# Kernel optimization log

Measured on AMD Instinct MI355X. Metric: run time of the kernel, lower is better.

## Reference

```python
import jax, jax.numpy as jnp
import numpy as np
from jax import lax

DIM = 192
HEADS = 8
EPS = 1e-5


def setup_inputs() -> dict:
    key = jax.random.key(0)
    ks = jax.random.split(key, 8)
    B, C, H, W = 1, DIM, 64, 64
    x = jax.random.normal(ks[0], (B, C, H, W), dtype=jnp.float32)
    gamma = jnp.ones((C,), dtype=jnp.float32)
    beta = jnp.zeros((C,), dtype=jnp.float32)
    w_qkv = jax.random.normal(ks[1], (3 * C, C), dtype=jnp.float32) * (1.0 / np.sqrt(C))
    # depthwise 3x3 conv: (out_ch=3C, in_ch/groups=1, 3, 3), bias present (Conv2d default)
    w_dw = jax.random.normal(ks[2], (3 * C, 1, 3, 3), dtype=jnp.float32) * (1.0 / 3.0)
    b_dw = jax.random.normal(ks[3], (3 * C,), dtype=jnp.float32) * 0.01
    w_proj = jax.random.normal(ks[4], (C, C), dtype=jnp.float32) * (1.0 / np.sqrt(C))
    temperature = jnp.ones((HEADS, 1, 1), dtype=jnp.float32)
    return {"x": x, "gamma": gamma, "beta": beta, "w_qkv": w_qkv,
            "w_dw": w_dw, "b_dw": b_dw, "w_proj": w_proj,
            "temperature": temperature}


def _mdta(x, gamma, beta, w_qkv, w_dw, b_dw, w_proj, temperature):
    B, C, H, W = x.shape
    heads = HEADS
    d = C // heads
    N = H * W
    # LayerNorm over channel dim (applied on NHWC permute in torch)
    mean = jnp.mean(x, axis=1, keepdims=True)
    var = jnp.var(x, axis=1, keepdims=True)
    x_ln = (x - mean) * lax.rsqrt(var + EPS)
    x_ln = x_ln * gamma[None, :, None, None] + beta[None, :, None, None]
    # 1x1 conv (no bias): [B,3C,H,W]
    qkv = jnp.einsum('oc,bchw->bohw', w_qkv, x_ln)
    # depthwise 3x3 conv, padding=1, groups=3C
    qkv = lax.conv_general_dilated(
        qkv, w_dw, window_strides=(1, 1), padding=((1, 1), (1, 1)),
        dimension_numbers=('NCHW', 'OIHW', 'NCHW'),
        feature_group_count=3 * C)
    qkv = qkv + b_dw[None, :, None, None]
    q, k, v = jnp.split(qkv, 3, axis=1)
    q = q.reshape(B, heads, d, N)
    k = k.reshape(B, heads, d, N)
    v = v.reshape(B, heads, d, N)
    # attn[b,h,n,m] = sum_d q[b,h,d,n] k[b,h,d,m], scaled by learnable temperature
    attn = jnp.einsum('bhdn,bhdm->bhnm', q, k) * temperature  # (heads,1,1) broadcasts
    attn = jax.nn.softmax(attn, axis=-1)
    # out[b,h,d,n] = sum_m attn[b,h,n,m] v[b,h,d,m]
    out = jnp.einsum('bhnm,bhdm->bhdn', attn, v)
    out = out.reshape(B, C, H, W)
    out = jnp.einsum('oc,bchw->bohw', w_proj, out)
    return out + x


def reference(x, gamma, beta, w_qkv, w_dw, b_dw, w_proj, temperature):
    return _mdta(x, gamma, beta, w_qkv, w_dw, b_dw, w_proj, temperature)
```

## Files before the change

kernel.cpp:

```cpp
#include <hip/hip_runtime.h>
#include <hip/hip_bf16.h>


typedef __bf16 bf16;
typedef __bf16 bf16x2 __attribute__((ext_vector_type(2)));
typedef __bf16 bf16x4 __attribute__((ext_vector_type(4)));
typedef __bf16 bf16x8 __attribute__((ext_vector_type(8)));
typedef float f32x4 __attribute__((ext_vector_type(4)));

#define C_DIM 192
#define N_PIX 4096
#define HEADS 8
#define DHEAD 24
#define DPAD 32
#define C3 576
#define NSPLIT 8

__device__ inline float fast_exp2(float x) {
#if __has_builtin(__builtin_amdgcn_exp2f)
    return __builtin_amdgcn_exp2f(x);
#else
    return exp2f(x);
#endif
}

__device__ inline f32x4 mfma16(bf16x8 a, bf16x8 b, f32x4 c) {
    return __builtin_amdgcn_mfma_f32_16x16x32_bf16(a, b, c, 0, 0, 0);
}

__global__ __launch_bounds__(256) void prep_ln(const float* __restrict__ x,
                                               const float* __restrict__ gamma,
                                               const float* __restrict__ beta,
                                               bf16* __restrict__ xln_t,
                                               const float* __restrict__ wqkv,
                                               const float* __restrict__ wproj,
                                               bf16* __restrict__ wqkv_b,
                                               bf16* __restrict__ wproj_b,
                                               float* __restrict__ maxk2) {
    int b = blockIdx.x, t = threadIdx.x;
    if (b >= 256) {
        int idx = (b - 256) * 256 + t;
        if (idx < C3 * C_DIM) wqkv_b[idx] = (bf16)wqkv[idx];
        if (idx < C_DIM * C_DIM) wproj_b[idx] = (bf16)wproj[idx];
        if (b == 256 && t < 8) maxk2[t] = 0.0f;
        return;
    }
    __shared__ float sred[256], ssred[256];
    int pixg = t & 15, cg = t >> 4;
    int p = b * 16 + pixg;
    float v[12];
    float s = 0.f, ss = 0.f;
    for (int j = 0; j < 12; ++j) {
        float f = x[(cg * 12 + j) * N_PIX + p];
        v[j] = f; s += f; ss += f * f;
    }
    sred[t] = s; ssred[t] = ss;
    __syncthreads();
    float S = 0.f, SS = 0.f;
    for (int k = 0; k < 16; ++k) { S += sred[k * 16 + pixg]; SS += ssred[k * 16 + pixg]; }
    float mean = S * (1.0f / C_DIM);
    float var = SS * (1.0f / C_DIM) - mean * mean;
    float rstd = rsqrtf(var + 1e-5f);
    for (int g = 0; g < 3; ++g) {
        bf16x4 w;
        for (int j = 0; j < 4; ++j) {
            int c = cg * 12 + g * 4 + j;
            w[j] = (bf16)((v[g * 4 + j] - mean) * rstd * gamma[c] + beta[c]);
        }
        *(bf16x4*)(xln_t + p * C_DIM + cg * 12 + g * 4) = w;
    }
}

__global__ __launch_bounds__(256) void gemm192(const bf16* __restrict__ A,
                                               const bf16* __restrict__ BT,
                                               bf16* __restrict__ outb) {
    const int K = 192;
    int n0 = blockIdx.x * 64;
    int m0 = blockIdx.y * 64;
    int tid = threadIdx.x;
    int wave = tid >> 6, lane = tid & 63;
    int l16 = lane & 15, quad = lane >> 4;
    int wm = (wave >> 1) * 32, wn = (wave & 1) * 32;
    f32x4 acc[2][2] = {};
    for (int kk = 0; kk < K; kk += 32) {
        bf16x8 a0 = *(const bf16x8*)(A + (m0 + wm + l16) * K + kk + quad * 8);
        bf16x8 a1 = *(const bf16x8*)(A + (m0 + wm + 16 + l16) * K + kk + quad * 8);
        bf16x8 b0 = *(const bf16x8*)(BT + (n0 + wn + l16) * K + kk + quad * 8);
        bf16x8 b1 = *(const bf16x8*)(BT + (n0 + wn + 16 + l16) * K + kk + quad * 8);
        acc[0][0] = mfma16(a0, b0, acc[0][0]);
        acc[0][1] = mfma16(a0, b1, acc[0][1]);
        acc[1][0] = mfma16(a1, b0, acc[1][0]);
        acc[1][1] = mfma16(a1, b1, acc[1][1]);
    }
    for (int i = 0; i < 2; ++i)
        for (int j = 0; j < 2; ++j)
            for (int r = 0; r < 4; ++r) {
                int row = m0 + wm + i * 16 + quad * 4 + r;
                int col = n0 + wn + j * 16 + l16;
                outb[row * N_PIX + col] = (bf16)acc[i][j][r];
            }
}

__global__ __launch_bounds__(256) void gemm_proj(const bf16* __restrict__ A,
                                                 const bf16* __restrict__ BT,
                                                 float* __restrict__ outf,
                                                 const float* __restrict__ resid) {
    const int K = 192;
    int n0 = blockIdx.x * 32;
    int m0 = blockIdx.y * 64;
    int tid = threadIdx.x;
    int wave = tid >> 6, lane = tid & 63;
    int l16 = lane & 15, quad = lane >> 4;
    int mrow = m0 + wave * 16;
    float rv[8];
    for (int j = 0; j < 2; ++j)
        for (int r = 0; r < 4; ++r)
            rv[j * 4 + r] = resid[(size_t)(mrow + quad * 4 + r) * N_PIX + n0 + j * 16 + l16];
    f32x4 acc[2] = {};
    for (int kk = 0; kk < K; kk += 32) {
        bf16x8 a = *(const bf16x8*)(A + (mrow + l16) * K + kk + quad * 8);
        bf16x8 b0 = *(const bf16x8*)(BT + (n0 + l16) * K + kk + quad * 8);
        bf16x8 b1 = *(const bf16x8*)(BT + (n0 + 16 + l16) * K + kk + quad * 8);
        acc[0] = mfma16(a, b0, acc[0]);
        acc[1] = mfma16(a, b1, acc[1]);
    }
    for (int j = 0; j < 2; ++j)
        for (int r = 0; r < 4; ++r) {
            int row = mrow + quad * 4 + r;
            int col = n0 + j * 16 + l16;
            outf[(size_t)row * N_PIX + col] = acc[j][r] + rv[j * 4 + r];
        }
}

__global__ __launch_bounds__(256) void dwconv(const bf16* __restrict__ qkv,
                                              const float* __restrict__ wdw,
                                              const float* __restrict__ bdw,
                                              bf16* __restrict__ qt,
                                              bf16* __restrict__ kt,
                                              bf16* __restrict__ vl,
                                              float* __restrict__ maxk2) {
    __shared__ float k2s[24][64];
    int bx = blockIdx.x;
    int part = bx >> 9;
    int h = (bx >> 6) & 7;
    int y = bx & 63;
    int t = threadIdx.x;
    int ch_local = t >> 3;
    int seg = t & 7;
    int px0 = seg * 8;
    bool active = ch_local < 24;

    float acc[8];
    if (active) {
        int ch = part * C_DIM + h * DHEAD + ch_local;
        const bf16* in = qkv + (size_t)ch * N_PIX;
        float w[9];
        for (int i = 0; i < 9; ++i) w[i] = wdw[ch * 9 + i];
        float bias = bdw[ch];
        float rowv[3][10];
        for (int r = 0; r < 3; ++r) {
            int yy = y + r - 1;
            if (yy >= 0 && yy < 64) {
                bf16x8 v8 = *(const bf16x8*)(in + yy * 64 + px0);
                for (int j = 0; j < 8; ++j) rowv[r][j + 1] = (float)v8[j];
                rowv[r][0] = (seg > 0) ? (float)in[yy * 64 + px0 - 1] : 0.f;
                rowv[r][9] = (seg < 7) ? (float)in[yy * 64 + px0 + 8] : 0.f;
            } else {
                for (int j = 0; j < 10; ++j) rowv[r][j] = 0.f;
            }
        }
        for (int j = 0; j < 8; ++j) {
            float a = bias;
            for (int r = 0; r < 3; ++r)
                a += w[r * 3 + 0] * rowv[r][j] + w[r * 3 + 1] * rowv[r][j + 1]
                   + w[r * 3 + 2] * rowv[r][j + 2];
            acc[j] = a;
        }
    }

    if (part == 2) {
        if (active) {
            bf16x8 v8;
            for (int j = 0; j < 8; ++j) v8[j] = (bf16)acc[j];
            *(bf16x8*)(vl + ((size_t)(h * DPAD + ch_local)) * N_PIX + y * 64 + px0) = v8;
        } else {
            int i = t - 192;
            int dd = 24 + (i >> 3);
            int s2 = i & 7;
            bf16 val = (bf16)((dd == 24) ? 1.0f : 0.0f);
            bf16x8 v8;
            for (int j = 0; j < 8; ++j) v8[j] = val;
            *(bf16x8*)(vl + ((size_t)(h * DPAD + dd)) * N_PIX + y * 64 + s2 * 8) = v8;
        }
    } else {
        bf16* dst = (part == 0 ? qt : kt) + ((size_t)h * N_PIX + y * 64) * DPAD;
        if (active) {
            for (int j = 0; j < 8; ++j)
                dst[(size_t)(px0 + j) * DPAD + ch_local] = (bf16)acc[j];
        } else {
            int i = t - 192;
            bf16x8 z;
            for (int j = 0; j < 8; ++j) z[j] = (bf16)0.0f;
            *(bf16x8*)(dst + (size_t)i * DPAD + 24) = z;
        }
        if (part == 1) {
            if (active)
                for (int j = 0; j < 8; ++j) k2s[ch_local][px0 + j] = acc[j] * acc[j];
            __syncthreads();
            if (t < 64) {
                float s = 0.f;
                for (int c = 0; c < 24; ++c) s += k2s[c][t];
                for (int off = 1; off < 64; off <<= 1)
                    s = fmaxf(s, __shfl_xor(s, off, 64));
                if (t == 0) atomicMax((unsigned int*)(maxk2 + h), __float_as_uint(s));
            }
        }
    }
}

__global__ __launch_bounds__(256, 4) void flash_attn(const bf16* __restrict__ qt,
                                                     const bf16* __restrict__ kt,
                                                     const bf16* __restrict__ vl,
                                                     const float* __restrict__ temp,
                                                     const float* __restrict__ maxk2,
                                                     bf16* __restrict__ opart,
                                                     bf16* __restrict__ lpart) {
    __shared__ __align__(16) bf16 Plds[4 * 4096];

    int tid = threadIdx.x;
    int wave = tid >> 6, lane = tid & 63;
    int l16 = lane & 15, quad = lane >> 4;
    int head = blockIdx.x & 7;
    int qb = (blockIdx.x >> 3) & 15;
    int split = blockIdx.x >> 7;
    int nbase = qb * 256 + wave * 64;
    float tl = temp[head] * 1.44269504f;

    const bf16* qrow = qt + ((size_t)head * N_PIX + nbase) * DPAD;
    bf16x8 aq[4];
    for (int f = 0; f < 4; ++f)
        aq[f] = *(const bf16x8*)(qrow + (size_t)(f * 16 + l16) * DPAD + quad * 8);

    float mk2 = maxk2[head];
    float Bb[4];
    for (int f = 0; f < 4; ++f) {
        float q2 = 0.f;
        for (int j = 0; j < 8; ++j) { float v = (float)aq[f][j]; q2 += v * v; }
        q2 += __shfl_xor(q2, 16, 64);
        q2 += __shfl_xor(q2, 32, 64);
        Bb[f] = fabsf(tl) * sqrtf(q2 * mk2) + 1.0f;
    }

    const bf16* kbase = kt + (size_t)head * N_PIX * DPAD;
    const bf16* vbase = vl + (size_t)head * DPAD * N_PIX;
    bf16* pw = Plds + wave * 4096;

    f32x4 o0[4] = {}, o1[4] = {};

    #pragma unroll 2
    for (int it = 0; it < 64 / NSPLIT; ++it) {
        int m0 = (split * (64 / NSPLIT) + it) * 64;
        bf16x8 ak[4];
        for (int mt = 0; mt < 4; ++mt)
            ak[mt] = *(const bf16x8*)(kbase + (size_t)(m0 + mt * 16 + l16) * DPAD + quad * 8);
        bf16x8 av[4];
        av[0] = *(const bf16x8*)(vbase + (size_t)l16 * N_PIX + m0 + quad * 8);
        av[1] = *(const bf16x8*)(vbase + (size_t)(16 + l16) * N_PIX + m0 + quad * 8);
        av[2] = *(const bf16x8*)(vbase + (size_t)l16 * N_PIX + m0 + 32 + quad * 8);
        av[3] = *(const bf16x8*)(vbase + (size_t)(16 + l16) * N_PIX + m0 + 32 + quad * 8);

        for (int f = 0; f < 4; ++f) {
            f32x4 z = {0.f, 0.f, 0.f, 0.f};
            f32x4 st[4];
            for (int mt = 0; mt < 4; ++mt) st[mt] = mfma16(ak[mt], aq[f], z);
            for (int mt = 0; mt < 4; ++mt) {
                bf16x4 pk;
                for (int r = 0; r < 4; ++r)
                    pk[r] = (bf16)fast_exp2(__builtin_fmaf(st[mt][r], tl, -Bb[f]));
                int chunk = mt * 2 + (quad >> 1);
                *(bf16x4*)(pw + f * 1024 + (chunk * 16 + l16) * 8 + (quad & 1) * 4) = pk;
            }
        }
        for (int f = 0; f < 4; ++f) {
            bf16x8 ap0 = *(const bf16x8*)(pw + f * 1024 + (quad * 16 + l16) * 8);
            bf16x8 ap1 = *(const bf16x8*)(pw + f * 1024 + ((4 + quad) * 16 + l16) * 8);
            o0[f] = mfma16(av[0], ap0, o0[f]);
            o1[f] = mfma16(av[1], ap0, o1[f]);
            o0[f] = mfma16(av[2], ap1, o0[f]);
            o1[f] = mfma16(av[3], ap1, o1[f]);
        }
    }

    for (int f = 0; f < 4; ++f) {
        int n = nbase + f * 16 + l16;
        size_t rowo = ((size_t)(split * 8 + head) * N_PIX + n) * 24;
        bf16x4 w0;
        for (int r = 0; r < 4; ++r) w0[r] = (bf16)o0[f][r];
        *(bf16x4*)(opart + rowo + quad * 4) = w0;
        if (quad < 2) {
            bf16x4 w1;
            for (int r = 0; r < 4; ++r) w1[r] = (bf16)o1[f][r];
            *(bf16x4*)(opart + rowo + 16 + quad * 4) = w1;
        }
        if (quad == 2)
            lpart[(size_t)(split * 8 + head) * N_PIX + n] = (bf16)o1[f][0];
    }
}

__global__ __launch_bounds__(256) void combine(const bf16* __restrict__ opart,
                                               const bf16* __restrict__ lpart,
                                               bf16* __restrict__ outt) {
    int idx = blockIdx.x * 256 + threadIdx.x;
    int n = idx & 4095;
    int h = idx >> 12;
    float acc[24];
    for (int j = 0; j < 24; ++j) acc[j] = 0.f;
    float l = 0.f;
    for (int s = 0; s < NSPLIT; ++s) {
        const bf16* row = opart + ((size_t)(s * 8 + h) * N_PIX + n) * 24;
        bf16x8 a = *(const bf16x8*)(row);
        bf16x8 b = *(const bf16x8*)(row + 8);
        bf16x8 c = *(const bf16x8*)(row + 16);
        for (int j = 0; j < 8; ++j) {
            acc[j] += (float)a[j];
            acc[8 + j] += (float)b[j];
            acc[16 + j] += (float)c[j];
        }
        l += (float)lpart[(size_t)(s * 8 + h) * N_PIX + n];
    }
    float inv = 1.0f / l;
    bf16* dst = outt + (size_t)n * C_DIM + h * DHEAD;
    for (int g = 0; g < 3; ++g) {
        bf16x8 w;
        for (int j = 0; j < 8; ++j) w[j] = (bf16)(acc[g * 8 + j] * inv);
        *(bf16x8*)(dst + g * 8) = w;
    }
}

extern "C" void kernel_launch(void* const* d_in, const int* in_sizes, int n_in,
                              void* d_out, int out_size, void* d_ws, size_t ws_size,
                              hipStream_t stream) {
    const float* x     = (const float*)d_in[0];
    const float* gamma = (const float*)d_in[1];
    const float* beta  = (const float*)d_in[2];
    const float* wqkv  = (const float*)d_in[3];
    const float* wdw   = (const float*)d_in[4];
    const float* bdw   = (const float*)d_in[5];
    const float* wproj = (const float*)d_in[6];
    const float* temp  = (const float*)d_in[7];
    float* out = (float*)d_out;

    char* ws = (char*)d_ws;
    bf16* wqkv_b  = (bf16*)(ws + 0);
    bf16* wproj_b = (bf16*)(ws + 221184);
    bf16* xln     = (bf16*)(ws + 294912);
    bf16* qkv     = (bf16*)(ws + 1867776);
    bf16* qt      = (bf16*)(ws + 6586368);
    bf16* kt      = (bf16*)(ws + 8683520);
    bf16* vl      = (bf16*)(ws + 10780672);
    bf16* opart   = (bf16*)(ws + 12877824);
    bf16* lpart   = (bf16*)(ws + 25460736);
    float* maxk2  = (float*)(ws + 25985024);
    bf16* outt    = qt;

    prep_ln<<<688, 256, 0, stream>>>(x, gamma, beta, xln, wqkv, wproj, wqkv_b, wproj_b, maxk2);
    gemm192<<<dim3(64, 9), 256, 0, stream>>>(wqkv_b, xln, qkv);
    dwconv<<<1536, 256, 0, stream>>>(qkv, wdw, bdw, qt, kt, vl, maxk2);
    flash_attn<<<NSPLIT * 128, 256, 0, stream>>>(qt, kt, vl, temp, maxk2, opart, lpart);
    combine<<<128, 256, 0, stream>>>(opart, lpart, outt);
    gemm_proj<<<dim3(128, 3), 256, 0, stream>>>(wproj_b, outt, out, x);
}
```

Baseline: 139.3 us.

## Fuse LayerNorm normalization into QKV GEMM operand load, keep only stats pass

The prep kernel now computes only per-pixel mean and rstd, with one thread per pixel looping over all 192 channels. It no longer writes a normalized bf16 transposed activation buffer. The QKV GEMM reads raw fp32 x directly, applies (x-mu)*rs*gamma+beta on the fly, and converts to bf16 for the MFMA B operand. This removes the intermediate xln write and read, but each GEMM block re-reads fp32 x, nine times across the M tiles. The B loads become strided scalar fp32 loads, and the stats pass runs only 16 blocks, which is low parallelism.

```diff
diff --git a/kernel.cpp b/kernel.cpp
--- a/kernel.cpp
+++ b/kernel.cpp
@@ -28,52 +28,41 @@
     return __builtin_amdgcn_mfma_f32_16x16x32_bf16(a, b, c, 0, 0, 0);
 }
 
-__global__ __launch_bounds__(256) void prep_ln(const float* __restrict__ x,
-                                               const float* __restrict__ gamma,
-                                               const float* __restrict__ beta,
-                                               bf16* __restrict__ xln_t,
-                                               const float* __restrict__ wqkv,
-                                               const float* __restrict__ wproj,
-                                               bf16* __restrict__ wqkv_b,
-                                               bf16* __restrict__ wproj_b,
-                                               float* __restrict__ maxk2) {
+__global__ __launch_bounds__(256) void prep(const float* __restrict__ x,
+                                            float* __restrict__ mu,
+                                            float* __restrict__ rs,
+                                            const float* __restrict__ wqkv,
+                                            const float* __restrict__ wproj,
+                                            bf16* __restrict__ wqkv_b,
+                                            bf16* __restrict__ wproj_b,
+                                            float* __restrict__ maxk2) {
     int b = blockIdx.x, t = threadIdx.x;
-    if (b >= 256) {
-        int idx = (b - 256) * 256 + t;
+    if (b >= 16) {
+        int idx = (b - 16) * 256 + t;
         if (idx < C3 * C_DIM) wqkv_b[idx] = (bf16)wqkv[idx];
         if (idx < C_DIM * C_DIM) wproj_b[idx] = (bf16)wproj[idx];
-        if (b == 256 && t < 8) maxk2[t] = 0.0f;
+        if (b == 16 && t < 8) maxk2[t] = 0.0f;
         return;
     }
-    __shared__ float sred[256], ssred[256];
-    int pixg = t & 15, cg = t >> 4;
-    int p = b * 16 + pixg;
-    float v[12];
+    int n = b * 256 + t;
     float s = 0.f, ss = 0.f;
-    for (int j = 0; j < 12; ++j) {
-        float f = x[(cg * 12 + j) * N_PIX + p];
-        v[j] = f; s += f; ss += f * f;
-    }
-    sred[t] = s; ssred[t] = ss;
-    __syncthreads();
-    float S = 0.f, SS = 0.f;
-    for (int k = 0; k < 16; ++k) { S += sred[k * 16 + pixg]; SS += ssred[k * 16 + pixg]; }
-    float mean = S * (1.0f / C_DIM);
-    float var = SS * (1.0f / C_DIM) - mean * mean;
-    float rstd = rsqrtf(var + 1e-5f);
-    for (int g = 0; g < 3; ++g) {
-        bf16x4 w;
-        for (int j = 0; j < 4; ++j) {
-            int c = cg * 12 + g * 4 + j;
-            w[j] = (bf16)((v[g * 4 + j] - mean) * rstd * gamma[c] + beta[c]);
-        }
-        *(bf16x4*)(xln_t + p * C_DIM + cg * 12 + g * 4) = w;
-    }
-}
-
-__global__ __launch_bounds__(256) void gemm192(const bf16* __restrict__ A,
-                                               const bf16* __restrict__ BT,
-                                               bf16* __restrict__ outb) {
+    for (int c = 0; c < C_DIM; ++c) {
+        float f = x[(size_t)c * N_PIX + n];
+        s += f; ss += f * f;
+    }
+    float mean = s * (1.0f / C_DIM);
+    float var = ss * (1.0f / C_DIM) - mean * mean;
+    mu[n] = mean;
+    rs[n] = rsqrtf(var + 1e-5f);
+}
+
+__global__ __launch_bounds__(256) void gemm192_ln(const bf16* __restrict__ A,
+                                                  const float* __restrict__ x,
+                                                  const float* __restrict__ mu,
+                                                  const float* __restrict__ rs,
+                                                  const float* __restrict__ gamma,
+                                                  const float* __restrict__ beta,
+                                                  bf16* __restrict__ outb) {
     const int K = 192;
     int n0 = blockIdx.x * 64;
     int m0 = blockIdx.y * 64;
@@ -81,23 +70,40 @@
     int wave = tid >> 6, lane = tid & 63;
     int l16 = lane & 15, quad = lane >> 4;
     int wm = (wave >> 1) * 32, wn = (wave & 1) * 32;
+    int nb0 = n0 + wn + l16, nb1 = nb0 + 16;
+    float a0n = rs[nb0], c0n = -mu[nb0] * a0n;
+    float a1n = rs[nb1], c1n = -mu[nb1] * a1n;
     f32x4 acc[2][2] = {};
     for (int kk = 0; kk < K; kk += 32) {
-        bf16x8 a0 = *(const bf16x8*)(A + (m0 + wm + l16) * K + kk + quad * 8);
-        bf16x8 a1 = *(const bf16x8*)(A + (m0 + wm + 16 + l16) * K + kk + quad * 8);
-        bf16x8 b0 = *(const bf16x8*)(BT + (n0 + wn + l16) * K + kk + quad * 8);
-        bf16x8 b1 = *(const bf16x8*)(BT + (n0 + wn + 16 + l16) * K + kk + quad * 8);
-        acc[0][0] = mfma16(a0, b0, acc[0][0]);
-        acc[0][1] = mfma16(a0, b1, acc[0][1]);
-        acc[1][0] = mfma16(a1, b0, acc[1][0]);
-        acc[1][1] = mfma16(a1, b1, acc[1][1]);
+        int k0 = kk + quad * 8;
+        float4 g0 = *(const float4*)(gamma + k0);
+        float4 g1 = *(const float4*)(gamma + k0 + 4);
+        float4 e0 = *(const float4*)(beta + k0);
+        float4 e1 = *(const float4*)(beta + k0 + 4);
+        float gk[8] = {g0.x, g0.y, g0.z, g0.w, g1.x, g1.y, g1.z, g1.w};
+        float ek[8] = {e0.x, e0.y, e0.z, e0.w, e1.x, e1.y, e1.z, e1.w};
+        bf16x8 b0f, b1f;
+        for (int j = 0; j < 8; ++j) {
+            float xv0 = x[(size_t)(k0 + j) * N_PIX + nb0];
+            float xv1 = x[(size_t)(k0 + j) * N_PIX + nb1];
+            float t0 = __builtin_fmaf(xv0, a0n, c0n);
+            float t1 = __builtin_fmaf(xv1, a1n, c1n);
+            b0f[j] = (bf16)__builtin_fmaf(t0, gk[j], ek[j]);
+            b1f[j] = (bf16)__builtin_fmaf(t1, gk[j], ek[j]);
+        }
+        bf16x8 a0 = *(const bf16x8*)(A + (m0 + wm + l16) * K + k0);
+        bf16x8 a1 = *(const bf16x8*)(A + (m0 + wm + 16 + l16) * K + k0);
+        acc[0][0] = mfma16(a0, b0f, acc[0][0]);
+        acc[0][1] = mfma16(a0, b1f, acc[0][1]);
+        acc[1][0] = mfma16(a1, b0f, acc[1][0]);
+        acc[1][1] = mfma16(a1, b1f, acc[1][1]);
     }
     for (int i = 0; i < 2; ++i)
         for (int j = 0; j < 2; ++j)
             for (int r = 0; r < 4; ++r) {
                 int row = m0 + wm + i * 16 + quad * 4 + r;
                 int col = n0 + wn + j * 16 + l16;
-                outb[row * N_PIX + col] = (bf16)acc[i][j][r];
+                outb[(size_t)row * N_PIX + col] = (bf16)acc[i][j][r];
             }
 }
 
@@ -353,18 +359,19 @@
     char* ws = (char*)d_ws;
     bf16* wqkv_b  = (bf16*)(ws + 0);
     bf16* wproj_b = (bf16*)(ws + 221184);
-    bf16* xln     = (bf16*)(ws + 294912);
-    bf16* qkv     = (bf16*)(ws + 1867776);
-    bf16* qt      = (bf16*)(ws + 6586368);
-    bf16* kt      = (bf16*)(ws + 8683520);
-    bf16* vl      = (bf16*)(ws + 10780672);
-    bf16* opart   = (bf16*)(ws + 12877824);
-    bf16* lpart   = (bf16*)(ws + 25460736);
-    float* maxk2  = (float*)(ws + 25985024);
+    float* mu     = (float*)(ws + 294912);
+    float* rs     = (float*)(ws + 311296);
+    bf16* qkv     = (bf16*)(ws + 327680);
+    bf16* qt      = (bf16*)(ws + 5046272);
+    bf16* kt      = (bf16*)(ws + 7143424);
+    bf16* vl      = (bf16*)(ws + 9240576);
+    bf16* opart   = (bf16*)(ws + 11337728);
+    bf16* lpart   = (bf16*)(ws + 23920640);
+    float* maxk2  = (float*)(ws + 24444928);
     bf16* outt    = qt;
 
-    prep_ln<<<688, 256, 0, stream>>>(x, gamma, beta, xln, wqkv, wproj, wqkv_b, wproj_b, maxk2);
-    gemm192<<<dim3(64, 9), 256, 0, stream>>>(wqkv_b, xln, qkv);
+    prep<<<448, 256, 0, stream>>>(x, mu, rs, wqkv, wproj, wqkv_b, wproj_b, maxk2);
+    gemm192_ln<<<dim3(64, 9), 256, 0, stream>>>(wqkv_b, x, mu, rs, gamma, beta, qkv);
     dwconv<<<1536, 256, 0, stream>>>(qkv, wdw, bdw, qt, kt, vl, maxk2);
     flash_attn<<<NSPLIT * 128, 256, 0, stream>>>(qt, kt, vl, temp, maxk2, opart, lpart);
     combine<<<128, 256, 0, stream>>>(opart, lpart, outt);
```

Result: slower. 144.3 us (+3.6%).
